# Kernel tuning notes

Measured on AMD Instinct MI355X. Metric: run time of the kernel, lower is better.

Reference implementation:

```python
import jax, jax.numpy as jnp
import numpy as np

B, D, H, E, NDIFF = 4096, 2048, 4096, 8, 3
TOPK = 2


def setup_inputs() -> dict:
    key = jax.random.key(0)
    ks = jax.random.split(key, 8)
    x = jax.random.normal(ks[0], (B, D), dtype=jnp.float32)
    difficulty_labels = jax.random.randint(ks[1], (B,), 0, NDIFF)
    emb = jax.random.normal(ks[2], (NDIFF, D), dtype=jnp.float32) * 0.02
    gate_W = jax.random.normal(ks[3], (E, 2 * D), dtype=jnp.float32) / np.sqrt(2.0 * D)
    gate_b = jnp.zeros((E,), dtype=jnp.float32)
    expert_W = jax.random.normal(ks[4], (E, H, D), dtype=jnp.float32) / np.sqrt(D)
    expert_b = jax.random.normal(ks[5], (E, H), dtype=jnp.float32) * 0.01
    return {"x": x, "difficulty_labels": difficulty_labels, "emb": emb,
            "gate_W": gate_W, "gate_b": gate_b,
            "expert_W": expert_W, "expert_b": expert_b}


def reference(x, difficulty_labels, emb, gate_W, gate_b, expert_W, expert_b):
    # gating: concat token features with difficulty embedding
    gate_in = jnp.concatenate([x, emb[difficulty_labels]], axis=1)       # [B, 2D]
    gate_logits = gate_in @ gate_W.T + gate_b                             # [B, E]
    topw, topk_idx = jax.lax.top_k(gate_logits, TOPK)                     # [B, 2]
    topk_probs = jax.nn.softmax(topw, axis=1)                             # [B, 2]
    # per-token combine weight for each expert (top-2 indices are distinct)
    combine = jnp.zeros((x.shape[0], E), dtype=x.dtype)
    combine = combine.at[jnp.arange(x.shape[0])[:, None], topk_idx].add(topk_probs)
    # dispatch/compute/combine: tokens with combine weight 0 contribute 0,
    # matching the masked gather/scatter-add of the original.
    out = jnp.zeros((x.shape[0], expert_W.shape[1]), dtype=x.dtype)
    for e in range(E):  # small fixed loop over experts
        y = x @ expert_W[e].T + expert_b[e]                               # [B, H]
        out = out + y * combine[:, e:e + 1]
    return (out, topk_idx)
```

## Files before the change

kernel.cpp:

```cpp
#include <hip/hip_runtime.h>
#include <hip/hip_bf16.h>

#define B_TOK 4096
#define DIM   2048
#define HID   4096
#define NEXP  8
#define CAP   4224

#define BM 128
#define BN 128
#define BK 32
#define KITER (DIM / BK)

typedef short  bf16x8 __attribute__((ext_vector_type(8)));
typedef unsigned short us16x8 __attribute__((ext_vector_type(8)));
typedef float  f32x4  __attribute__((ext_vector_type(4)));

__device__ __forceinline__ unsigned short f2bf(float f) {
    unsigned u = __builtin_bit_cast(unsigned, f);
    u += 0x7fffu + ((u >> 16) & 1u);
    return (unsigned short)(u >> 16);
}

__device__ __forceinline__ void async_copy16(const void* g, void* l) {
    __builtin_amdgcn_global_load_lds(
        (const __attribute__((address_space(1))) unsigned*)g,
        (__attribute__((address_space(3))) unsigned*)l, 16, 0, 0);
}

__global__ __launch_bounds__(256) void cvt_kernel(
    const float* __restrict__ src, unsigned short* __restrict__ dst, long n) {
    long i = ((long)blockIdx.x * 256 + threadIdx.x) * 8;
    if (i >= n) return;
    float4 v0 = *(const float4*)(src + i);
    float4 v1 = *(const float4*)(src + i + 4);
    us16x8 o = { f2bf(v0.x), f2bf(v0.y), f2bf(v0.z), f2bf(v0.w),
                 f2bf(v1.x), f2bf(v1.y), f2bf(v1.z), f2bf(v1.w) };
    *(us16x8*)(dst + i) = o;
}

__global__ __launch_bounds__(256) void compute_c_kernel(
    const float* __restrict__ emb, const float* __restrict__ gate_W,
    const float* __restrict__ gate_b, float* __restrict__ cbuf) {
    int wave = (blockIdx.x * blockDim.x + threadIdx.x) >> 6;
    int lane = threadIdx.x & 63;
    if (wave >= 24) return;
    int n = wave >> 3, e = wave & 7;
    const float4* er = (const float4*)(emb + (size_t)n * DIM);
    const float4* wr = (const float4*)(gate_W + (size_t)e * 2 * DIM + DIM);
    float acc = 0.f;
    for (int c = lane; c < DIM / 4; c += 64) {
        float4 a = er[c], b = wr[c];
        acc += a.x * b.x + a.y * b.y + a.z * b.z + a.w * b.w;
    }
    #pragma unroll
    for (int off = 32; off; off >>= 1) acc += __shfl_down(acc, off, 64);
    if (lane == 0) cbuf[n * 8 + e] = acc + gate_b[e];
}

__global__ __launch_bounds__(256) void gating_kernel(
    const float* __restrict__ x, const int* __restrict__ labels,
    const float* __restrict__ gate_W, const float* __restrict__ cbuf,
    int* __restrict__ counts, int* __restrict__ tlist, int* __restrict__ rlist,
    float* __restrict__ wA, float* __restrict__ wB,
    int* __restrict__ eA, int* __restrict__ eB,
    float* __restrict__ out_idx) {
    int wave = threadIdx.x >> 6, lane = threadIdx.x & 63;
    int b = blockIdx.x * 4 + wave;
    const float4* xr  = (const float4*)(x + (size_t)b * DIM);
    const float4* gw4 = (const float4*)gate_W;
    float acc[8] = {0.f, 0.f, 0.f, 0.f, 0.f, 0.f, 0.f, 0.f};
    for (int c = lane; c < DIM / 4; c += 64) {
        float4 xv = xr[c];
        #pragma unroll
        for (int e = 0; e < 8; ++e) {
            float4 wv = gw4[e * (2 * DIM / 4) + c];
            acc[e] += xv.x * wv.x + xv.y * wv.y + xv.z * wv.z + xv.w * wv.w;
        }
    }
    #pragma unroll
    for (int off = 32; off; off >>= 1) {
        #pragma unroll
        for (int e = 0; e < 8; ++e) acc[e] += __shfl_down(acc[e], off, 64);
    }
    if (lane == 0) {
        int lbl = labels[b];
        float lg[8];
        #pragma unroll
        for (int e = 0; e < 8; ++e) lg[e] = acc[e] + cbuf[lbl * 8 + e];
        int e0 = 0; float t0 = lg[0];
        #pragma unroll
        for (int e = 1; e < 8; ++e) if (lg[e] > t0) { t0 = lg[e]; e0 = e; }
        int e1 = -1; float t1 = -1e30f;
        #pragma unroll
        for (int e = 0; e < 8; ++e)
            if (e != e0 && lg[e] > t1) { t1 = lg[e]; e1 = e; }
        float w0 = 1.f / (1.f + __expf(t1 - t0));
        float w1 = 1.f - w0;
        int p0 = atomicAdd(&counts[e0], 1);
        int p1 = atomicAdd(&counts[e1], 1);
        tlist[e0 * CAP + p0] = b; rlist[e0 * CAP + p0] = 0;
        tlist[e1 * CAP + p1] = b; rlist[e1 * CAP + p1] = 1;
        wA[b] = w0; wB[b] = w1; eA[b] = e0; eB[b] = e1;
        out_idx[2 * b]     = (float)e0;
        out_idx[2 * b + 1] = (float)e1;
    }
}

__global__ void pad_kernel(const int* __restrict__ counts,
                           int* __restrict__ tlist, int* __restrict__ rlist) {
    int e = blockIdx.x, c = counts[e];
    int padded = (c + BM - 1) & ~(BM - 1);
    int i = c + threadIdx.x;
    if (i < padded) { tlist[e * CAP + i] = 0; rlist[e * CAP + i] = 2; }
}

__global__ __launch_bounds__(256, 3) void moe_gemm_kernel(
    const unsigned short* __restrict__ xb, const unsigned short* __restrict__ Wb,
    const int* __restrict__ counts, const int* __restrict__ tlist,
    const int* __restrict__ rlist,
    float* __restrict__ out0, float* __restrict__ y1, float* __restrict__ trash) {
    const int e  = blockIdx.z;
    const int m0 = blockIdx.y * BM;
    if (m0 >= counts[e]) return;
    const int n0 = blockIdx.x * BN;

    __shared__ unsigned short As0[BM * BK], As1[BM * BK];
    __shared__ unsigned short Bs0[BN * BK], Bs1[BN * BK];
    __shared__ int toks[BM];
    __shared__ unsigned long long rowp[BM];

    const int t = threadIdx.x;
    if (t < BM) {
        int tok = tlist[e * CAP + m0 + t];
        int rk  = rlist[e * CAP + m0 + t];
        toks[t] = tok;
        float* p = (rk == 0) ? out0 + (size_t)tok * HID
                 : (rk == 1) ? y1   + (size_t)tok * HID
                             : trash;
        rowp[t] = (unsigned long long)p;
    }
    __syncthreads();

    const int lane = t & 63, wave = t >> 6;
    const int rowc = lane >> 2;
    const int colg = lane & 3;
    const int gcol = ((colg ^ (rowc & 3)) * 8);

    const unsigned short* gA[2];
    const unsigned short* gB[2];
    int ldsoff[2];
    #pragma unroll
    for (int j = 0; j < 2; ++j) {
        int row = wave * 32 + j * 16 + rowc;
        gA[j] = xb + (size_t)toks[row] * DIM + gcol;
        gB[j] = Wb + ((size_t)e * HID + n0 + row) * DIM + gcol;
        ldsoff[j] = (wave * 32 + j * 16) * BK;
    }

    const int wm = wave >> 1, wn = wave & 1;
    const int r = lane & 15, quad = lane >> 4;
    const int pg = (quad ^ (r & 3)) * 8;

    f32x4 acc[4][4] = {};

    auto stage = [&](unsigned short* Ad, unsigned short* Bd, int kstep) {
        const int kc = kstep * BK;
        #pragma unroll
        for (int j = 0; j < 2; ++j) {
            async_copy16(gA[j] + kc, Ad + ldsoff[j]);
            async_copy16(gB[j] + kc, Bd + ldsoff[j]);
        }
    };
    auto compute = [&](const unsigned short* Ab, const unsigned short* Bb) {
        bf16x8 af[4], bfr[4];
        #pragma unroll
        for (int i = 0; i < 4; ++i) {
            af[i]  = *(const bf16x8*)&Ab[(wm * 64 + i * 16 + r) * BK + pg];
            bfr[i] = *(const bf16x8*)&Bb[(wn * 64 + i * 16 + r) * BK + pg];
        }
        #pragma unroll
        for (int im = 0; im < 4; ++im)
            #pragma unroll
            for (int in = 0; in < 4; ++in)
                acc[im][in] = __builtin_amdgcn_mfma_f32_16x16x32_bf16(
                    af[im], bfr[in], acc[im][in], 0, 0, 0);
    };

    stage(As0, Bs0, 0);
    __syncthreads();
    for (int k2 = 0; k2 < KITER; k2 += 2) {
        stage(As1, Bs1, k2 + 1);
        compute(As0, Bs0);
        __syncthreads();
        if (k2 + 2 < KITER) stage(As0, Bs0, k2 + 2);
        compute(As1, Bs1);
        __syncthreads();
    }

    #pragma unroll
    for (int in = 0; in < 4; ++in) {
        int col = n0 + wn * 64 + in * 16 + r;
        #pragma unroll
        for (int im = 0; im < 4; ++im) {
            int rowb = wm * 64 + im * 16 + quad * 4;
            #pragma unroll
            for (int r4 = 0; r4 < 4; ++r4) {
                float* dst = (float*)rowp[rowb + r4];
                dst[col] = acc[im][in][r4];
            }
        }
    }
}

__global__ __launch_bounds__(256) void combine_kernel(
    const float* __restrict__ y1, const float* __restrict__ eb,
    const float* __restrict__ wA, const float* __restrict__ wB,
    const int* __restrict__ eA, const int* __restrict__ eB,
    float* __restrict__ out) {
    int b = blockIdx.x;
    float w0 = wA[b], w1 = wB[b];
    int e0 = eA[b], e1 = eB[b];
    const float4* y0r = (const float4*)(out + (size_t)b * HID);
    const float4* y1r = (const float4*)(y1 + (size_t)b * HID);
    const float4* b0r = (const float4*)(eb + (size_t)e0 * HID);
    const float4* b1r = (const float4*)(eb + (size_t)e1 * HID);
    float4* o = (float4*)(out + (size_t)b * HID);
    for (int i = threadIdx.x; i < HID / 4; i += 256) {
        float4 a = y0r[i], c = y1r[i], u = b0r[i], v = b1r[i];
        float4 rs;
        rs.x = w0 * (a.x + u.x) + w1 * (c.x + v.x);
        rs.y = w0 * (a.y + u.y) + w1 * (c.y + v.y);
        rs.z = w0 * (a.z + u.z) + w1 * (c.z + v.z);
        rs.w = w0 * (a.w + u.w) + w1 * (c.w + v.w);
        o[i] = rs;
    }
}

extern "C" void kernel_launch(void* const* d_in, const int* in_sizes, int n_in,
                              void* d_out, int out_size, void* d_ws, size_t ws_size,
                              hipStream_t stream) {
    const float* x        = (const float*)d_in[0];
    const int*   labels   = (const int*)  d_in[1];
    const float* emb      = (const float*)d_in[2];
    const float* gate_W   = (const float*)d_in[3];
    const float* gate_b   = (const float*)d_in[4];
    const float* expert_W = (const float*)d_in[5];
    const float* expert_b = (const float*)d_in[6];
    float* out = (float*)d_out;

    char* ws = (char*)d_ws;
    int*   counts = (int*)ws;
    float* cbuf   = (float*)(ws + 256);
    int*   tlist  = (int*)(ws + 512);
    int*   rlist  = (int*)(ws + 512 + 135168);
    float* wA     = (float*)(ws + 270848);
    float* wB     = (float*)(ws + 287232);
    int*   eA     = (int*)  (ws + 303616);
    int*   eB     = (int*)  (ws + 320000);
    float* trash  = (float*)(ws + 336384);
    float* y1     = (float*)(ws + 352768);
    unsigned short* xb = (unsigned short*)(ws + 352768 + (size_t)B_TOK * HID * 4);
    unsigned short* Wb = xb + (size_t)B_TOK * DIM;

    hipMemsetAsync(counts, 0, 8 * sizeof(int), stream);

    cvt_kernel<<<(B_TOK * DIM) / (8 * 256), 256, 0, stream>>>(
        x, xb, (long)B_TOK * DIM);
    cvt_kernel<<<(NEXP * HID * DIM) / (8 * 256), 256, 0, stream>>>(
        expert_W, Wb, (long)NEXP * HID * DIM);
    compute_c_kernel<<<6, 256, 0, stream>>>(emb, gate_W, gate_b, cbuf);
    gating_kernel<<<B_TOK / 4, 256, 0, stream>>>(
        x, labels, gate_W, cbuf, counts, tlist, rlist, wA, wB, eA, eB,
        out + (size_t)B_TOK * HID);
    pad_kernel<<<NEXP, BM, 0, stream>>>(counts, tlist, rlist);
    moe_gemm_kernel<<<dim3(HID / BN, B_TOK / BM, NEXP), 256, 0, stream>>>(
        xb, Wb, counts, tlist, rlist, out, y1, trash);
    combine_kernel<<<B_TOK, 256, 0, stream>>>(
        y1, expert_b, wA, wB, eA, eB, out);
}
```

Before: 756.5 us.

## Enlarge MoE GEMM tiles, triple-buffer loads, fuse combine and bias into atomic epilogue

The expert GEMM now uses 256x256 tiles with 512 threads and a three-slot LDS ring, with prefetch split around the MFMA blocks and raised wave priority during MFMA. This is meant to increase operand reuse and hide global-load latency. The separate combine pass and y1 buffer are removed: the epilogue adds the bias, scales by the gate weight and atomically accumulates into a zeroed output. The fp32-to-bf16 conversion of x is folded into the gating kernel. In exchange it adds a full-output memset, float atomics on every output element, and LDS use that likely allows only one block per CU.

Result: slower. 947.4 us (+25.2%).

```diff
diff --git a/kernel.cpp b/kernel.cpp
--- a/kernel.cpp
+++ b/kernel.cpp
@@ -5,10 +5,10 @@
 #define DIM   2048
 #define HID   4096
 #define NEXP  8
-#define CAP   4224
-
-#define BM 128
-#define BN 128
+#define CAP   4096
+
+#define BM 256
+#define BN 256
 #define BK 32
 #define KITER (DIM / BK)
 
@@ -63,15 +63,17 @@
     const float* __restrict__ gate_W, const float* __restrict__ cbuf,
     int* __restrict__ counts, int* __restrict__ tlist, int* __restrict__ rlist,
     float* __restrict__ wA, float* __restrict__ wB,
-    int* __restrict__ eA, int* __restrict__ eB,
-    float* __restrict__ out_idx) {
+    unsigned short* __restrict__ xb, float* __restrict__ out_idx) {
     int wave = threadIdx.x >> 6, lane = threadIdx.x & 63;
     int b = blockIdx.x * 4 + wave;
     const float4* xr  = (const float4*)(x + (size_t)b * DIM);
     const float4* gw4 = (const float4*)gate_W;
+    unsigned short* xo = xb + (size_t)b * DIM;
     float acc[8] = {0.f, 0.f, 0.f, 0.f, 0.f, 0.f, 0.f, 0.f};
     for (int c = lane; c < DIM / 4; c += 64) {
         float4 xv = xr[c];
+        ushort4 xc = { f2bf(xv.x), f2bf(xv.y), f2bf(xv.z), f2bf(xv.w) };
+        *(ushort4*)(xo + 4 * c) = xc;
         #pragma unroll
         for (int e = 0; e < 8; ++e) {
             float4 wv = gw4[e * (2 * DIM / 4) + c];
@@ -101,7 +103,7 @@
         int p1 = atomicAdd(&counts[e1], 1);
         tlist[e0 * CAP + p0] = b; rlist[e0 * CAP + p0] = 0;
         tlist[e1 * CAP + p1] = b; rlist[e1 * CAP + p1] = 1;
-        wA[b] = w0; wB[b] = w1; eA[b] = e0; eB[b] = e1;
+        wA[b] = w0; wB[b] = w1;
         out_idx[2 * b]     = (float)e0;
         out_idx[2 * b + 1] = (float)e1;
     }
@@ -115,19 +117,21 @@
     if (i < padded) { tlist[e * CAP + i] = 0; rlist[e * CAP + i] = 2; }
 }
 
-__global__ __launch_bounds__(256, 3) void moe_gemm_kernel(
+__global__ __launch_bounds__(512, 2) void moe_gemm_kernel(
     const unsigned short* __restrict__ xb, const unsigned short* __restrict__ Wb,
     const int* __restrict__ counts, const int* __restrict__ tlist,
-    const int* __restrict__ rlist,
-    float* __restrict__ out0, float* __restrict__ y1, float* __restrict__ trash) {
+    const int* __restrict__ rlist, const float* __restrict__ wA,
+    const float* __restrict__ wB, const float* __restrict__ eb,
+    float* __restrict__ out) {
     const int e  = blockIdx.z;
     const int m0 = blockIdx.y * BM;
     if (m0 >= counts[e]) return;
     const int n0 = blockIdx.x * BN;
 
-    __shared__ unsigned short As0[BM * BK], As1[BM * BK];
-    __shared__ unsigned short Bs0[BN * BK], Bs1[BN * BK];
-    __shared__ int toks[BM];
+    __shared__ unsigned short Abuf[3][BM * BK];
+    __shared__ unsigned short Bbuf[3][BN * BK];
+    __shared__ int   toks[BM];
+    __shared__ float roww[BM];
     __shared__ unsigned long long rowp[BM];
 
     const int t = threadIdx.x;
@@ -135,105 +139,106 @@
         int tok = tlist[e * CAP + m0 + t];
         int rk  = rlist[e * CAP + m0 + t];
         toks[t] = tok;
-        float* p = (rk == 0) ? out0 + (size_t)tok * HID
-                 : (rk == 1) ? y1   + (size_t)tok * HID
-                             : trash;
-        rowp[t] = (unsigned long long)p;
+        roww[t] = (rk == 0) ? wA[tok] : (rk == 1) ? wB[tok] : 0.f;
+        rowp[t] = (unsigned long long)(out + (size_t)tok * HID);
     }
     __syncthreads();
 
-    const int lane = t & 63, wave = t >> 6;
-    const int rowc = lane >> 2;
-    const int colg = lane & 3;
-    const int gcol = ((colg ^ (rowc & 3)) * 8);
-
-    const unsigned short* gA[2];
-    const unsigned short* gB[2];
-    int ldsoff[2];
-    #pragma unroll
-    for (int j = 0; j < 2; ++j) {
-        int row = wave * 32 + j * 16 + rowc;
-        gA[j] = xb + (size_t)toks[row] * DIM + gcol;
-        gB[j] = Wb + ((size_t)e * HID + n0 + row) * DIM + gcol;
-        ldsoff[j] = (wave * 32 + j * 16) * BK;
-    }
-
-    const int wm = wave >> 1, wn = wave & 1;
+    const int lane = t & 63, wv = t >> 6;
     const int r = lane & 15, quad = lane >> 4;
-    const int pg = (quad ^ (r & 3)) * 8;
-
-    f32x4 acc[4][4] = {};
-
-    auto stage = [&](unsigned short* Ad, unsigned short* Bd, int kstep) {
-        const int kc = kstep * BK;
-        #pragma unroll
-        for (int j = 0; j < 2; ++j) {
-            async_copy16(gA[j] + kc, Ad + ldsoff[j]);
-            async_copy16(gB[j] + kc, Bd + ldsoff[j]);
-        }
+    const int wm = wv >> 2, wn = wv & 3;
+
+    const unsigned short* gAsrc[2];
+    const unsigned short* gBsrc[2];
+    int ldsc[2];
+    #pragma unroll
+    for (int s = 0; s < 2; ++s) {
+        int chunk = s * 512 + t;
+        int row   = chunk >> 2;
+        int csrc  = ((chunk & 3) << 4) ^ ((row & 3) << 4);
+        gAsrc[s] = xb + (size_t)toks[row] * DIM + (csrc >> 1);
+        gBsrc[s] = Wb + ((size_t)e * HID + n0 + row) * DIM + (csrc >> 1);
+        ldsc[s]  = (s * 512 + wv * 64) * 8;
+    }
+
+    auto stage_half = [&](int slot, int kt, int s) {
+        const int kc = kt * BK;
+        async_copy16(gAsrc[s] + kc, &Abuf[slot][ldsc[s]]);
+        async_copy16(gBsrc[s] + kc, &Bbuf[slot][ldsc[s]]);
     };
-    auto compute = [&](const unsigned short* Ab, const unsigned short* Bb) {
-        bf16x8 af[4], bfr[4];
-        #pragma unroll
-        for (int i = 0; i < 4; ++i) {
-            af[i]  = *(const bf16x8*)&Ab[(wm * 64 + i * 16 + r) * BK + pg];
-            bfr[i] = *(const bf16x8*)&Bb[(wn * 64 + i * 16 + r) * BK + pg];
-        }
-        #pragma unroll
-        for (int im = 0; im < 4; ++im)
+
+    const int fOff = (quad * 16) ^ ((r & 3) << 4);
+    f32x4 acc[8][4] = {};
+
+    stage_half(0, 0, 0); stage_half(0, 0, 1);
+    stage_half(1, 1, 0); stage_half(1, 1, 1);
+    asm volatile("s_waitcnt vmcnt(4)" ::: "memory");
+    __builtin_amdgcn_s_barrier();
+    __builtin_amdgcn_sched_barrier(0);
+
+    int slot = 0, slot2 = 2;
+    for (int kt = 0; kt < KITER; ++kt) {
+        const bool pf = (kt + 2 < KITER);
+        if (pf) stage_half(slot2, kt + 2, 0);
+
+        const char* Ab = (const char*)&Abuf[slot][0];
+        const char* Bb = (const char*)&Bbuf[slot][0];
+        bf16x8 a[4], b[4];
+        #pragma unroll
+        for (int i = 0; i < 4; ++i)
+            a[i] = *(const bf16x8*)(Ab + (wm * 128 + i * 16 + r) * 64 + fOff);
+        #pragma unroll
+        for (int j = 0; j < 4; ++j)
+            b[j] = *(const bf16x8*)(Bb + (wn * 64 + j * 16 + r) * 64 + fOff);
+        __builtin_amdgcn_s_setprio(1);
+        #pragma unroll
+        for (int i = 0; i < 4; ++i)
             #pragma unroll
-            for (int in = 0; in < 4; ++in)
-                acc[im][in] = __builtin_amdgcn_mfma_f32_16x16x32_bf16(
-                    af[im], bfr[in], acc[im][in], 0, 0, 0);
-    };
-
-    stage(As0, Bs0, 0);
-    __syncthreads();
-    for (int k2 = 0; k2 < KITER; k2 += 2) {
-        stage(As1, Bs1, k2 + 1);
-        compute(As0, Bs0);
-        __syncthreads();
-        if (k2 + 2 < KITER) stage(As0, Bs0, k2 + 2);
-        compute(As1, Bs1);
-        __syncthreads();
-    }
-
-    #pragma unroll
-    for (int in = 0; in < 4; ++in) {
-        int col = n0 + wn * 64 + in * 16 + r;
-        #pragma unroll
-        for (int im = 0; im < 4; ++im) {
-            int rowb = wm * 64 + im * 16 + quad * 4;
+            for (int j = 0; j < 4; ++j)
+                acc[i][j] = __builtin_amdgcn_mfma_f32_16x16x32_bf16(
+                    a[i], b[j], acc[i][j], 0, 0, 0);
+        __builtin_amdgcn_s_setprio(0);
+
+        if (pf) stage_half(slot2, kt + 2, 1);
+
+        bf16x8 a2[4];
+        #pragma unroll
+        for (int i = 0; i < 4; ++i)
+            a2[i] = *(const bf16x8*)(Ab + (wm * 128 + (i + 4) * 16 + r) * 64 + fOff);
+        __builtin_amdgcn_s_setprio(1);
+        #pragma unroll
+        for (int i = 0; i < 4; ++i)
+            #pragma unroll
+            for (int j = 0; j < 4; ++j)
+                acc[i + 4][j] = __builtin_amdgcn_mfma_f32_16x16x32_bf16(
+                    a2[i], b[j], acc[i + 4][j], 0, 0, 0);
+        __builtin_amdgcn_s_setprio(0);
+
+        __builtin_amdgcn_sched_barrier(0);
+        if (pf) asm volatile("s_waitcnt vmcnt(4)" ::: "memory");
+        else    asm volatile("s_waitcnt vmcnt(0)" ::: "memory");
+        __builtin_amdgcn_s_barrier();
+        __builtin_amdgcn_sched_barrier(0);
+
+        slot  = (slot  == 2) ? 0 : slot  + 1;
+        slot2 = (slot2 == 2) ? 0 : slot2 + 1;
+    }
+
+    #pragma unroll
+    for (int j = 0; j < 4; ++j) {
+        int col = n0 + wn * 64 + j * 16 + r;
+        float bc = eb[(size_t)e * HID + col];
+        #pragma unroll
+        for (int i = 0; i < 8; ++i) {
+            int rowb = wm * 128 + i * 16 + quad * 4;
             #pragma unroll
             for (int r4 = 0; r4 < 4; ++r4) {
-                float* dst = (float*)rowp[rowb + r4];
-                dst[col] = acc[im][in][r4];
+                float w = roww[rowb + r4];
+                if (w != 0.f)
+                    atomicAdd((float*)rowp[rowb + r4] + col,
+                              w * (acc[i][j][r4] + bc));
             }
         }
-    }
-}
-
-__global__ __launch_bounds__(256) void combine_kernel(
-    const float* __restrict__ y1, const float* __restrict__ eb,
-    const float* __restrict__ wA, const float* __restrict__ wB,
-    const int* __restrict__ eA, const int* __restrict__ eB,
-    float* __restrict__ out) {
-    int b = blockIdx.x;
-    float w0 = wA[b], w1 = wB[b];
-    int e0 = eA[b], e1 = eB[b];
-    const float4* y0r = (const float4*)(out + (size_t)b * HID);
-    const float4* y1r = (const float4*)(y1 + (size_t)b * HID);
-    const float4* b0r = (const float4*)(eb + (size_t)e0 * HID);
-    const float4* b1r = (const float4*)(eb + (size_t)e1 * HID);
-    float4* o = (float4*)(out + (size_t)b * HID);
-    for (int i = threadIdx.x; i < HID / 4; i += 256) {
-        float4 a = y0r[i], c = y1r[i], u = b0r[i], v = b1r[i];
-        float4 rs;
-        rs.x = w0 * (a.x + u.x) + w1 * (c.x + v.x);
-        rs.y = w0 * (a.y + u.y) + w1 * (c.y + v.y);
-        rs.z = w0 * (a.z + u.z) + w1 * (c.z + v.z);
-        rs.w = w0 * (a.w + u.w) + w1 * (c.w + v.w);
-        o[i] = rs;
     }
 }
 
@@ -253,29 +258,22 @@
     int*   counts = (int*)ws;
     float* cbuf   = (float*)(ws + 256);
     int*   tlist  = (int*)(ws + 512);
-    int*   rlist  = (int*)(ws + 512 + 135168);
-    float* wA     = (float*)(ws + 270848);
-    float* wB     = (float*)(ws + 287232);
-    int*   eA     = (int*)  (ws + 303616);
-    int*   eB     = (int*)  (ws + 320000);
-    float* trash  = (float*)(ws + 336384);
-    float* y1     = (float*)(ws + 352768);
-    unsigned short* xb = (unsigned short*)(ws + 352768 + (size_t)B_TOK * HID * 4);
+    int*   rlist  = (int*)(ws + 512 + 131072);
+    float* wA     = (float*)(ws + 262656);
+    float* wB     = (float*)(ws + 279040);
+    unsigned short* xb = (unsigned short*)(ws + 295424);
     unsigned short* Wb = xb + (size_t)B_TOK * DIM;
 
     hipMemsetAsync(counts, 0, 8 * sizeof(int), stream);
-
-    cvt_kernel<<<(B_TOK * DIM) / (8 * 256), 256, 0, stream>>>(
-        x, xb, (long)B_TOK * DIM);
+    hipMemsetAsync(out, 0, (size_t)B_TOK * HID * sizeof(float), stream);
+
     cvt_kernel<<<(NEXP * HID * DIM) / (8 * 256), 256, 0, stream>>>(
         expert_W, Wb, (long)NEXP * HID * DIM);
     compute_c_kernel<<<6, 256, 0, stream>>>(emb, gate_W, gate_b, cbuf);
     gating_kernel<<<B_TOK / 4, 256, 0, stream>>>(
-        x, labels, gate_W, cbuf, counts, tlist, rlist, wA, wB, eA, eB,
+        x, labels, gate_W, cbuf, counts, tlist, rlist, wA, wB, xb,
         out + (size_t)B_TOK * HID);
     pad_kernel<<<NEXP, BM, 0, stream>>>(counts, tlist, rlist);
-    moe_gemm_kernel<<<dim3(HID / BN, B_TOK / BM, NEXP), 256, 0, stream>>>(
-        xb, Wb, counts, tlist, rlist, out, y1, trash);
-    combine_kernel<<<B_TOK, 256, 0, stream>>>(
-        y1, expert_b, wA, wB, eA, eB, out);
-}
+    moe_gemm_kernel<<<dim3(HID / BN, B_TOK / BM, NEXP), 512, 0, stream>>>(
+        xb, Wb, counts, tlist, rlist, wA, wB, expert_b, out);
+}
```
